# Performance work log

Hardware: AMD Instinct MI355X
Metric: run time of the kernel (lower is better)

Reference implementation:

```python
import jax, jax.numpy as jnp
import numpy as np

B, L, E, V = 4, 2048, 1024, 64
NT = V * (V - 1) // 2  # 2016 upper-triangular entries
LN_EPS = 1e-5


def setup_inputs() -> dict:
    key = jax.random.key(0)
    ks = jax.random.split(key, 9)
    s = lambda d: 1.0 / np.sqrt(d)
    return {
        "hx": jax.random.normal(ks[0], (B, L, E), dtype=jnp.float32),
        "W_dense": jax.random.normal(ks[1], (E, E), dtype=jnp.float32) * s(E),
        "b_dense": jnp.zeros((E,), dtype=jnp.float32),
        "ln_g": jnp.ones((E,), dtype=jnp.float32),
        "ln_b": jnp.zeros((E,), dtype=jnp.float32),
        "W_theta": jax.random.normal(ks[2], (V, E), dtype=jnp.float32) * s(E),
        "b_theta": jnp.zeros((V,), dtype=jnp.float32),
        "W_Theta": jax.random.normal(ks[3], (NT, E), dtype=jnp.float32) * s(E),
        "b_Theta": jnp.zeros((NT,), dtype=jnp.float32),
    }


def reference(hx, W_dense, b_dense, ln_g, ln_b, W_theta, b_theta, W_Theta, b_Theta):
    # dense -> exact (erf) gelu -> LayerNorm (ESM1bLayerNorm)
    h = jax.nn.gelu(hx @ W_dense.T + b_dense, approximate=False)
    mu = jnp.mean(h, axis=-1, keepdims=True)
    var = jnp.mean(jnp.square(h - mu), axis=-1, keepdims=True)
    h = (h - mu) / jnp.sqrt(var + LN_EPS) * ln_g + ln_b

    pi = jax.nn.softmax(h @ W_theta.T + b_theta, axis=-1)          # (B,L,V)
    Theta = jax.nn.softplus(h @ W_Theta.T + b_Theta)               # (B,L,NT)

    iu, ju = np.triu_indices(V, k=1)
    S = jnp.zeros((B, L, V, V), dtype=h.dtype).at[:, :, iu, ju].set(Theta)
    S = S + jnp.swapaxes(S, -2, -1)                                # symmetric, zero diag

    # diag(1/sqrt(pi)) @ S @ diag(sqrt(pi)) == S * sqrt(pi_j)/sqrt(pi_i)
    pi_sqrt = jnp.sqrt(pi)
    Q = S * (pi_sqrt[..., None, :] / pi_sqrt[..., :, None])
    Q = Q - Q.sum(axis=-1)[..., :, None] * jnp.eye(V, dtype=Q.dtype)
    return (Q, pi)
```

## Files before the change

### kernel.cpp

```cpp
#include <hip/hip_runtime.h>
#include <hip/hip_bf16.h>
#include <cstdint>
#include <cstddef>

#define MROWS 8192
#define EDIM  1024
#define VDIM  64
#define NTRI  2016
#define NTC   2176

typedef _Float16 half8  __attribute__((ext_vector_type(8)));
typedef _Float16 half4v __attribute__((ext_vector_type(4)));
typedef float    floatx4 __attribute__((ext_vector_type(4)));

typedef __attribute__((address_space(1))) void gvoid;
typedef __attribute__((address_space(3))) void svoid;

__device__ inline void gld_lds16(const _Float16* g, _Float16* l) {
    __builtin_amdgcn_global_load_lds((gvoid*)g, (svoid*)l, 16, 0, 0);
}

__device__ inline float fast_erf(float x) {
    float ax = fabsf(x);
    float t = 1.0f / (1.0f + 0.3275911f * ax);
    float p = t * (0.254829592f +
              t * (-0.284496736f +
              t * (1.421413741f +
              t * (-1.453152027f +
              t * 1.061405429f))));
    float r = 1.0f - p * __expf(-ax * ax);
    return copysignf(r, x);
}

__device__ inline float fast_softplus(float x) {
    return fmaxf(x, 0.0f) + __logf(1.0f + __expf(-fabsf(x)));
}

__global__ __launch_bounds__(256) void cast_all(const float* __restrict__ hx,
                                                const float* __restrict__ Wd,
                                                const float* __restrict__ WT,
                                                const float* __restrict__ wt,
                                                _Float16* __restrict__ A_h,
                                                _Float16* __restrict__ Wd_h,
                                                _Float16* __restrict__ Wc_h) {
    const int b = blockIdx.x;
    float4 v;
    _Float16* dst;
    int idx;
    if (b < 8192) {
        idx = (b * 256 + threadIdx.x) * 4;
        v = *(const float4*)(hx + idx);
        dst = A_h;
    } else if (b < 9216) {
        idx = ((b - 8192) * 256 + threadIdx.x) * 4;
        v = *(const float4*)(Wd + idx);
        dst = Wd_h;
    } else {
        idx = ((b - 9216) * 256 + threadIdx.x) * 4;
        if (idx < NTRI * EDIM)                  v = *(const float4*)(WT + idx);
        else if (idx < (NTRI + VDIM) * EDIM)    v = *(const float4*)(wt + (idx - NTRI * EDIM));
        else                                    v = make_float4(0.f, 0.f, 0.f, 0.f);
        dst = Wc_h;
    }
    half4v o;
    o[0] = (_Float16)v.x; o[1] = (_Float16)v.y;
    o[2] = (_Float16)v.z; o[3] = (_Float16)v.w;
    *(half4v*)(dst + idx) = o;
}

template <int MODE>
__global__ __launch_bounds__(256, 3) void gemm128(const _Float16* __restrict__ A,
                                                  const _Float16* __restrict__ Bt,
                                                  const float* __restrict__ bias,
                                                  const float* __restrict__ bias2,
                                                  _Float16* __restrict__ C,
                                                  int ldC, int ntg) {
    constexpr int NT = EDIM / 32;
    __shared__ __align__(16) _Float16 S[3][8192];

    const int tid  = threadIdx.x;
    const int xcd  = blockIdx.x & 7;
    const int slot = blockIdx.x >> 3;
    const int mg   = slot / ntg;
    const int nn   = slot - mg * ntg;
    const int m0   = (xcd + mg * 8) * 128;
    const int n0   = nn * 128;

    const int w = tid >> 6, lane = tid & 63;
    const int wr = w >> 1, wc = w & 1;
    const int lrow = lane & 15, lquad = lane >> 4;

    floatx4 acc[4][4] = {};

    const int r0 = tid >> 2;
    const int c0 = tid & 3;
    const int gk = (c0 ^ ((r0 >> 1) & 3)) * 8;
    const _Float16* Ag0 = A  + (size_t)(m0 + r0) * EDIM + gk;
    const _Float16* Ag1 = Ag0 + (size_t)64 * EDIM;
    const _Float16* Bg0 = Bt + (size_t)(n0 + r0) * EDIM + gk;
    const _Float16* Bg1 = Bg0 + (size_t)64 * EDIM;

    const int xr   = (lrow >> 1) & 3;
    const int koff = (lquad ^ xr) * 8;
    const int aoff = (wr * 64 + lrow) * 32 + koff;
    const int boff = 4096 + (wc * 64 + lrow) * 32 + koff;

    auto stage = [&](int buf, int kt) {
        _Float16* d = &S[buf][tid * 8];
        const int ko = kt * 32;
        gld_lds16(Ag0 + ko, d);
        gld_lds16(Ag1 + ko, d + 2048);
        gld_lds16(Bg0 + ko, d + 4096);
        gld_lds16(Bg1 + ko, d + 6144);
    };

    stage(0, 0);
    stage(1, 1);
    asm volatile("s_waitcnt vmcnt(4)" ::: "memory");
    __builtin_amdgcn_s_barrier();

    int buf = 0, sbuf = 2;
#pragma unroll 1
    for (int t = 0; t < NT; ++t) {
        const _Float16* Sb = S[buf];
        if (t + 2 < NT) stage(sbuf, t + 2);

        half8 af[4], bf[4];
#pragma unroll
        for (int i = 0; i < 4; ++i) af[i] = *(const half8*)(Sb + aoff + i * 512);
#pragma unroll
        for (int j = 0; j < 4; ++j) bf[j] = *(const half8*)(Sb + boff + j * 512);

        __builtin_amdgcn_s_setprio(1);
#pragma unroll
        for (int i = 0; i < 4; ++i)
#pragma unroll
            for (int j = 0; j < 4; ++j)
                acc[i][j] = __builtin_amdgcn_mfma_f32_16x16x32_f16(
                    af[i], bf[j], acc[i][j], 0, 0, 0);
        __builtin_amdgcn_s_setprio(0);

        if (t < NT - 2)       asm volatile("s_waitcnt vmcnt(4)" ::: "memory");
        else if (t == NT - 2) asm volatile("s_waitcnt vmcnt(0)" ::: "memory");
        if (t < NT - 1) {
            asm volatile("" ::: "memory");
            __builtin_amdgcn_s_barrier();
            asm volatile("" ::: "memory");
        }
        buf  = (buf  == 2) ? 0 : buf + 1;
        sbuf = (sbuf == 2) ? 0 : sbuf + 1;
    }

    const int cm = m0 + wr * 64 + lquad * 4;
    const int cn = n0 + wc * 64 + lrow;
#pragma unroll
    for (int j = 0; j < 4; ++j) {
        const int gn = cn + j * 16;
        float bv;
        if (MODE == 0) {
            bv = bias[gn];
        } else {
            if (gn < NTRI)             bv = bias[gn];
            else if (gn < NTRI + VDIM) bv = bias2[gn - NTRI];
            else                       bv = 0.0f;
        }
#pragma unroll
        for (int i = 0; i < 4; ++i) {
#pragma unroll
            for (int r = 0; r < 4; ++r) {
                float x = acc[i][j][r] + bv;
                float y;
                if (MODE == 0) {
                    y = 0.5f * x * (1.0f + fast_erf(x * 0.70710678118654752f));
                } else {
                    if (gn < NTRI)             y = fast_softplus(x);
                    else if (gn < NTRI + VDIM) y = x;
                    else                       y = 0.0f;
                }
                C[(size_t)(cm + i * 16 + r) * ldC + gn] = (_Float16)y;
            }
        }
    }
}

__global__ __launch_bounds__(256) void ln_kernel(const _Float16* __restrict__ G,
                                                 const float* __restrict__ gw,
                                                 const float* __restrict__ bw,
                                                 _Float16* __restrict__ Hh) {
    const int row = blockIdx.x, tid = threadIdx.x;
    half4v v = ((const half4v*)(G + (size_t)row * EDIM))[tid];
    float x0 = (float)v[0], x1 = (float)v[1], x2 = (float)v[2], x3 = (float)v[3];
    float s  = x0 + x1 + x2 + x3;
    float ss = x0 * x0 + x1 * x1 + x2 * x2 + x3 * x3;
#pragma unroll
    for (int off = 32; off; off >>= 1) {
        s  += __shfl_down(s, off);
        ss += __shfl_down(ss, off);
    }
    __shared__ float red[8];
    const int w = tid >> 6, lane = tid & 63;
    if (lane == 0) { red[w] = s; red[4 + w] = ss; }
    __syncthreads();
    const float st  = red[0] + red[1] + red[2] + red[3];
    const float sst = red[4] + red[5] + red[6] + red[7];
    const float mu  = st * (1.0f / EDIM);
    const float rs  = 1.0f / sqrtf(sst * (1.0f / EDIM) - mu * mu + 1e-5f);
    float4 gg = ((const float4*)gw)[tid];
    float4 bb = ((const float4*)bw)[tid];
    half4v h4;
    h4[0] = (_Float16)((x0 - mu) * rs * gg.x + bb.x);
    h4[1] = (_Float16)((x1 - mu) * rs * gg.y + bb.y);
    h4[2] = (_Float16)((x2 - mu) * rs * gg.z + bb.z);
    h4[3] = (_Float16)((x3 - mu) * rs * gg.w + bb.w);
    ((half4v*)(Hh + (size_t)row * EDIM))[tid] = h4;
}

__global__ __launch_bounds__(256) void q_kernel(const _Float16* __restrict__ Theta,
                                                float* __restrict__ pi_out,
                                                float* __restrict__ Q) {
    const int row = blockIdx.x;
    const int tid = threadIdx.x;
    __shared__ float Th[NTRI];
    __shared__ float spv[VDIM];
    const _Float16* trow = Theta + (size_t)row * NTC;
    if (tid < 252) {
        half8 h = *(const half8*)(trow + tid * 8);
#pragma unroll
        for (int u = 0; u < 8; ++u) Th[tid * 8 + u] = (float)h[u];
    }
    if (tid >= 192) {
        const int lane = tid & 63;
        float lg = (float)trow[NTRI + lane];
        float m = lg;
#pragma unroll
        for (int off = 32; off; off >>= 1) m = fmaxf(m, __shfl_xor(m, off));
        float e = __expf(lg - m);
        float ssum = e;
#pragma unroll
        for (int off = 32; off; off >>= 1) ssum += __shfl_xor(ssum, off);
        float p = e / ssum;
        pi_out[(size_t)row * VDIM + lane] = p;
        spv[lane] = sqrtf(p);
    }
    __syncthreads();

    const int i = tid >> 2;
    const int q = tid & 3;
    const float rpi = 1.0f / spv[i];
    float vals[16];
    float psum = 0.f;
#pragma unroll
    for (int c = 0; c < 16; ++c) {
        const int j = q * 16 + c;
        float out = 0.f;
        if (j != i) {
            const int a = (i < j) ? i : j;
            const int b = (i < j) ? j : i;
            const int t = a * (127 - a) / 2 + (b - a - 1);
            out = Th[t] * spv[j] * rpi;
            psum += out;
        }
        vals[c] = out;
    }
    psum += __shfl_xor(psum, 1);
    psum += __shfl_xor(psum, 2);
    if ((i >> 4) == q) vals[i & 15] = -psum;

    float* qrow = Q + ((size_t)row * VDIM + i) * VDIM + q * 16;
    float4* dst = (float4*)qrow;
    dst[0] = make_float4(vals[0], vals[1], vals[2], vals[3]);
    dst[1] = make_float4(vals[4], vals[5], vals[6], vals[7]);
    dst[2] = make_float4(vals[8], vals[9], vals[10], vals[11]);
    dst[3] = make_float4(vals[12], vals[13], vals[14], vals[15]);
}

extern "C" void kernel_launch(void* const* d_in, const int* in_sizes, int n_in,
                              void* d_out, int out_size, void* d_ws, size_t ws_size,
                              hipStream_t stream) {
    const float* hx      = (const float*)d_in[0];
    const float* W_dense = (const float*)d_in[1];
    const float* b_dense = (const float*)d_in[2];
    const float* ln_g    = (const float*)d_in[3];
    const float* ln_b    = (const float*)d_in[4];
    const float* W_theta = (const float*)d_in[5];
    const float* b_theta = (const float*)d_in[6];
    const float* W_Theta = (const float*)d_in[7];
    const float* b_Theta = (const float*)d_in[8];

    uint8_t* ws = (uint8_t*)d_ws;
    _Float16* A_h  = (_Float16*)ws;
    _Float16* Wd_h = (_Float16*)(ws + (size_t)16 * 1048576);
    _Float16* Wc_h = (_Float16*)(ws + (size_t)18 * 1048576);
    _Float16* G_h  = (_Float16*)(ws + (size_t)23 * 1048576);
    _Float16* Th_h = (_Float16*)(ws + (size_t)23 * 1048576);

    float* Q_out  = (float*)d_out;
    float* pi_out = (float*)d_out + (size_t)MROWS * VDIM * VDIM;

    cast_all<<<11392, 256, 0, stream>>>(hx, W_dense, W_Theta, W_theta,
                                        A_h, Wd_h, Wc_h);

    gemm128<0><<<512, 256, 0, stream>>>(A_h, Wd_h, b_dense, nullptr, G_h, EDIM, 8);

    ln_kernel<<<MROWS, 256, 0, stream>>>(G_h, ln_g, ln_b, A_h);

    gemm128<1><<<1088, 256, 0, stream>>>(A_h, Wc_h, b_Theta, b_theta, Th_h, NTC, 17);

    q_kernel<<<MROWS, 256, 0, stream>>>(Th_h, pi_out, Q_out);
}
```

Baseline: 307.7 us.

## Replace 128x128 GEMM with 256x128 tile, 8-wave, BK=64 phased pipeline

```diff
diff --git a/kernel.cpp b/kernel.cpp
--- a/kernel.cpp
+++ b/kernel.cpp
@@ -19,6 +19,8 @@
 __device__ inline void gld_lds16(const _Float16* g, _Float16* l) {
     __builtin_amdgcn_global_load_lds((gvoid*)g, (svoid*)l, 16, 0, 0);
 }
+
+#define MFMA16(a, b, c) __builtin_amdgcn_mfma_f32_16x16x32_f16((a), (b), (c), 0, 0, 0)
 
 __device__ inline float fast_erf(float x) {
     float ax = fabsf(x);
@@ -69,92 +71,119 @@
 }
 
 template <int MODE>
-__global__ __launch_bounds__(256, 3) void gemm128(const _Float16* __restrict__ A,
+__global__ __launch_bounds__(512, 2) void gemm256(const _Float16* __restrict__ A,
                                                   const _Float16* __restrict__ Bt,
                                                   const float* __restrict__ bias,
                                                   const float* __restrict__ bias2,
                                                   _Float16* __restrict__ C,
                                                   int ldC, int ntg) {
-    constexpr int NT = EDIM / 32;
-    __shared__ __align__(16) _Float16 S[3][8192];
+    __shared__ __align__(16) _Float16 S[2][24576];
 
     const int tid  = threadIdx.x;
     const int xcd  = blockIdx.x & 7;
     const int slot = blockIdx.x >> 3;
     const int mg   = slot / ntg;
     const int nn   = slot - mg * ntg;
-    const int m0   = (xcd + mg * 8) * 128;
+    const int m0   = (xcd + mg * 8) * 256;
     const int n0   = nn * 128;
 
     const int w = tid >> 6, lane = tid & 63;
-    const int wr = w >> 1, wc = w & 1;
+    const int wr = w >> 2;
+    const int wc = w & 3;
     const int lrow = lane & 15, lquad = lane >> 4;
 
-    floatx4 acc[4][4] = {};
-
-    const int r0 = tid >> 2;
-    const int c0 = tid & 3;
-    const int gk = (c0 ^ ((r0 >> 1) & 3)) * 8;
-    const _Float16* Ag0 = A  + (size_t)(m0 + r0) * EDIM + gk;
-    const _Float16* Ag1 = Ag0 + (size_t)64 * EDIM;
-    const _Float16* Bg0 = Bt + (size_t)(n0 + r0) * EDIM + gk;
-    const _Float16* Bg1 = Bg0 + (size_t)64 * EDIM;
-
-    const int xr   = (lrow >> 1) & 3;
-    const int koff = (lquad ^ xr) * 8;
-    const int aoff = (wr * 64 + lrow) * 32 + koff;
-    const int boff = 4096 + (wc * 64 + lrow) * 32 + koff;
-
-    auto stage = [&](int buf, int kt) {
-        _Float16* d = &S[buf][tid * 8];
-        const int ko = kt * 32;
-        gld_lds16(Ag0 + ko, d);
-        gld_lds16(Ag1 + ko, d + 2048);
-        gld_lds16(Bg0 + ko, d + 4096);
-        gld_lds16(Bg1 + ko, d + 6144);
+    floatx4 acc[8][2] = {};
+
+    const int sr = tid >> 3;
+    const int sc = tid & 7;
+    const int gk = (sc ^ (sr & 7)) * 8;
+    const _Float16* pA = A  + (size_t)(m0 + sr) * EDIM + gk;
+    const _Float16* pB = Bt + (size_t)(n0 + sr) * EDIM + gk;
+
+    const int k0off = ( lquad      ^ (lrow & 7)) * 8;
+    const int k1off = ((4 + lquad) ^ (lrow & 7)) * 8;
+    const int abase = (wr * 128 + lrow) * 64;
+    const int bbase = 16384 + (wc * 32 + lrow) * 64;
+
+    auto stA = [&](int buf, int kt, int seg) {
+        gld_lds16(pA + (size_t)seg * 64 * EDIM + kt * 64,
+                  &S[buf][seg * 4096 + tid * 8]);
     };
-
-    stage(0, 0);
-    stage(1, 1);
-    asm volatile("s_waitcnt vmcnt(4)" ::: "memory");
+    auto stB = [&](int buf, int kt, int seg) {
+        gld_lds16(pB + (size_t)seg * 64 * EDIM + kt * 64,
+                  &S[buf][16384 + seg * 4096 + tid * 8]);
+    };
+
+    half8 bf[4];
+    auto loadB = [&](const _Float16* Sb) {
+        bf[0] = *(const half8*)(Sb + bbase + k0off);
+        bf[1] = *(const half8*)(Sb + bbase + k1off);
+        bf[2] = *(const half8*)(Sb + bbase + 1024 + k0off);
+        bf[3] = *(const half8*)(Sb + bbase + 1024 + k1off);
+    };
+
+#define PHASE(SB, P, STAGE_STMT, TAIL_STMT)                                   \
+    {                                                                         \
+        const _Float16* Sb_ = (SB);                                           \
+        half8 a00 = *(const half8*)(Sb_ + abase + (2*(P))*1024   + k0off);    \
+        half8 a01 = *(const half8*)(Sb_ + abase + (2*(P))*1024   + k1off);    \
+        half8 a10 = *(const half8*)(Sb_ + abase + (2*(P)+1)*1024 + k0off);    \
+        half8 a11 = *(const half8*)(Sb_ + abase + (2*(P)+1)*1024 + k1off);    \
+        STAGE_STMT;                                                           \
+        asm volatile("" ::: "memory");                                        \
+        __builtin_amdgcn_s_barrier();                                         \
+        asm volatile("" ::: "memory");                                        \
+        __builtin_amdgcn_s_setprio(1);                                        \
+        acc[2*(P)][0]   = MFMA16(a00, bf[0], acc[2*(P)][0]);                  \
+        acc[2*(P)][0]   = MFMA16(a01, bf[1], acc[2*(P)][0]);                  \
+        acc[2*(P)][1]   = MFMA16(a00, bf[2], acc[2*(P)][1]);                  \
+        acc[2*(P)][1]   = MFMA16(a01, bf[3], acc[2*(P)][1]);                  \
+        acc[2*(P)+1][0] = MFMA16(a10, bf[0], acc[2*(P)+1][0]);                \
+        acc[2*(P)+1][0] = MFMA16(a11, bf[1], acc[2*(P)+1][0]);                \
+        acc[2*(P)+1][1] = MFMA16(a10, bf[2], acc[2*(P)+1][1]);                \
+        acc[2*(P)+1][1] = MFMA16(a11, bf[3], acc[2*(P)+1][1]);                \
+        __builtin_amdgcn_s_setprio(0);                                        \
+        TAIL_STMT;                                                            \
+        asm volatile("" ::: "memory");                                        \
+        __builtin_amdgcn_s_barrier();                                         \
+        asm volatile("" ::: "memory");                                        \
+    }
+
+    stA(0, 0, 0); stA(0, 0, 1); stA(0, 0, 2); stA(0, 0, 3);
+    stB(0, 0, 0); stB(0, 0, 1);
+    stB(1, 1, 0); stB(1, 1, 1);
+    asm volatile("s_waitcnt vmcnt(2)" ::: "memory");
     __builtin_amdgcn_s_barrier();
-
-    int buf = 0, sbuf = 2;
+    asm volatile("" ::: "memory");
+
 #pragma unroll 1
-    for (int t = 0; t < NT; ++t) {
-        const _Float16* Sb = S[buf];
-        if (t + 2 < NT) stage(sbuf, t + 2);
-
-        half8 af[4], bf[4];
-#pragma unroll
-        for (int i = 0; i < 4; ++i) af[i] = *(const half8*)(Sb + aoff + i * 512);
-#pragma unroll
-        for (int j = 0; j < 4; ++j) bf[j] = *(const half8*)(Sb + boff + j * 512);
-
-        __builtin_amdgcn_s_setprio(1);
-#pragma unroll
-        for (int i = 0; i < 4; ++i)
-#pragma unroll
-            for (int j = 0; j < 4; ++j)
-                acc[i][j] = __builtin_amdgcn_mfma_f32_16x16x32_f16(
-                    af[i], bf[j], acc[i][j], 0, 0, 0);
-        __builtin_amdgcn_s_setprio(0);
-
-        if (t < NT - 2)       asm volatile("s_waitcnt vmcnt(4)" ::: "memory");
-        else if (t == NT - 2) asm volatile("s_waitcnt vmcnt(0)" ::: "memory");
-        if (t < NT - 1) {
-            asm volatile("" ::: "memory");
-            __builtin_amdgcn_s_barrier();
-            asm volatile("" ::: "memory");
-        }
-        buf  = (buf  == 2) ? 0 : buf + 1;
-        sbuf = (sbuf == 2) ? 0 : sbuf + 1;
-    }
-
-    const int cm = m0 + wr * 64 + lquad * 4;
-    const int cn = n0 + wc * 64 + lrow;
-#pragma unroll
-    for (int j = 0; j < 4; ++j) {
+    for (int it = 0; it < 8; ++it) {
+        const int t0 = 2 * it, t1 = 2 * it + 1;
+        const bool st = (it < 7);
+        const _Float16* S0 = S[0];
+        const _Float16* S1 = S[1];
+
+        loadB(S0);
+        PHASE(S0, 0, { stA(1, t1, 0); stA(1, t1, 1); }, {});
+        PHASE(S0, 1, { stA(1, t1, 2); stA(1, t1, 3); }, {});
+        PHASE(S0, 2, { if (st) stB(0, t0 + 2, 0); }, {});
+        PHASE(S0, 3, { if (st) stB(0, t0 + 2, 1); },
+              { if (st) asm volatile("s_waitcnt vmcnt(2)" ::: "memory");
+                else    asm volatile("s_waitcnt vmcnt(0)" ::: "memory"); });
+
+        loadB(S1);
+        PHASE(S1, 0, { if (st) { stA(0, t0 + 2, 0); stA(0, t0 + 2, 1); } }, {});
+        PHASE(S1, 1, { if (st) { stA(0, t0 + 2, 2); stA(0, t0 + 2, 3); } }, {});
+        PHASE(S1, 2, { if (st) stB(1, t1 + 2, 0); }, {});
+        PHASE(S1, 3, { if (st) stB(1, t1 + 2, 1); },
+              { if (st) asm volatile("s_waitcnt vmcnt(2)" ::: "memory"); });
+    }
+#undef PHASE
+
+    const int cm = m0 + wr * 128 + lquad * 4;
+    const int cn = n0 + wc * 32 + lrow;
+#pragma unroll
+    for (int j = 0; j < 2; ++j) {
         const int gn = cn + j * 16;
         float bv;
         if (MODE == 0) {
@@ -165,7 +194,7 @@
             else                       bv = 0.0f;
         }
 #pragma unroll
-        for (int i = 0; i < 4; ++i) {
+        for (int i = 0; i < 8; ++i) {
 #pragma unroll
             for (int r = 0; r < 4; ++r) {
                 float x = acc[i][j][r] + bv;
@@ -300,11 +329,11 @@
     cast_all<<<11392, 256, 0, stream>>>(hx, W_dense, W_Theta, W_theta,
                                         A_h, Wd_h, Wc_h);
 
-    gemm128<0><<<512, 256, 0, stream>>>(A_h, Wd_h, b_dense, nullptr, G_h, EDIM, 8);
+    gemm256<0><<<256, 512, 0, stream>>>(A_h, Wd_h, b_dense, nullptr, G_h, EDIM, 8);
 
     ln_kernel<<<MROWS, 256, 0, stream>>>(G_h, ln_g, ln_b, A_h);
 
-    gemm128<1><<<1088, 256, 0, stream>>>(A_h, Wc_h, b_Theta, b_theta, Th_h, NTC, 17);
+    gemm256<1><<<544, 512, 0, stream>>>(A_h, Wc_h, b_Theta, b_theta, Th_h, NTC, 17);
 
     q_kernel<<<MROWS, 256, 0, stream>>>(Th_h, pi_out, Q_out);
 }
```

New measurement: 314.1 us. 2.1% more time.

## Widen GEMM tiles to 128x256 with 512-thread blocks and mixed-width tail

Applied to the files above, without the earlier changes.

```diff
diff --git a/kernel.cpp b/kernel.cpp
--- a/kernel.cpp
+++ b/kernel.cpp
@@ -19,6 +19,8 @@
 __device__ inline void gld_lds16(const _Float16* g, _Float16* l) {
     __builtin_amdgcn_global_load_lds((gvoid*)g, (svoid*)l, 16, 0, 0);
 }
+
+#define MFMA16(a, b, c) __builtin_amdgcn_mfma_f32_16x16x32_f16((a), (b), (c), 0, 0, 0)
 
 __device__ inline float fast_erf(float x) {
     float ax = fabsf(x);
@@ -68,55 +70,54 @@
     *(half4v*)(dst + idx) = o;
 }
 
-template <int MODE>
-__global__ __launch_bounds__(256, 3) void gemm128(const _Float16* __restrict__ A,
-                                                  const _Float16* __restrict__ Bt,
-                                                  const float* __restrict__ bias,
-                                                  const float* __restrict__ bias2,
-                                                  _Float16* __restrict__ C,
-                                                  int ldC, int ntg) {
+template <int MODE, int BNF>
+__device__ inline void gemm_body(const _Float16* __restrict__ A,
+                                 const _Float16* __restrict__ Bt,
+                                 const float* __restrict__ bias,
+                                 const float* __restrict__ bias2,
+                                 _Float16* __restrict__ C,
+                                 int ldC, int ntg, int bidx, int col0,
+                                 _Float16 (*S)[12288]) {
     constexpr int NT = EDIM / 32;
-    __shared__ __align__(16) _Float16 S[3][8192];
+    constexpr int BN = BNF * 64;
 
     const int tid  = threadIdx.x;
-    const int xcd  = blockIdx.x & 7;
-    const int slot = blockIdx.x >> 3;
+    const int xcd  = bidx & 7;
+    const int slot = bidx >> 3;
     const int mg   = slot / ntg;
     const int nn   = slot - mg * ntg;
     const int m0   = (xcd + mg * 8) * 128;
-    const int n0   = nn * 128;
+    const int n0   = col0 + nn * BN;
 
     const int w = tid >> 6, lane = tid & 63;
-    const int wr = w >> 1, wc = w & 1;
+    const int wr = w >> 2, wc = w & 3;
     const int lrow = lane & 15, lquad = lane >> 4;
 
-    floatx4 acc[4][4] = {};
+    floatx4 acc[4][BNF] = {};
 
     const int r0 = tid >> 2;
     const int c0 = tid & 3;
     const int gk = (c0 ^ ((r0 >> 1) & 3)) * 8;
-    const _Float16* Ag0 = A  + (size_t)(m0 + r0) * EDIM + gk;
-    const _Float16* Ag1 = Ag0 + (size_t)64 * EDIM;
+    const _Float16* Ag  = A  + (size_t)(m0 + r0) * EDIM + gk;
     const _Float16* Bg0 = Bt + (size_t)(n0 + r0) * EDIM + gk;
-    const _Float16* Bg1 = Bg0 + (size_t)64 * EDIM;
+    const _Float16* Bg1 = Bg0 + (size_t)128 * EDIM;
 
     const int xr   = (lrow >> 1) & 3;
     const int koff = (lquad ^ xr) * 8;
     const int aoff = (wr * 64 + lrow) * 32 + koff;
-    const int boff = 4096 + (wc * 64 + lrow) * 32 + koff;
+    const int boff = 4096 + (wc * (BNF * 16) + lrow) * 32 + koff;
 
     auto stage = [&](int buf, int kt) {
-        _Float16* d = &S[buf][tid * 8];
         const int ko = kt * 32;
-        gld_lds16(Ag0 + ko, d);
-        gld_lds16(Ag1 + ko, d + 2048);
-        gld_lds16(Bg0 + ko, d + 4096);
-        gld_lds16(Bg1 + ko, d + 6144);
+        gld_lds16(Ag + ko, &S[buf][tid * 8]);
+        gld_lds16(Bg0 + ko, &S[buf][4096 + tid * 8]);
+        if constexpr (BNF == 4) gld_lds16(Bg1 + ko, &S[buf][8192 + tid * 8]);
     };
 
     stage(0, 0);
     stage(1, 1);
-    asm volatile("s_waitcnt vmcnt(4)" ::: "memory");
+    if constexpr (BNF == 4) asm volatile("s_waitcnt vmcnt(3)" ::: "memory");
+    else                    asm volatile("s_waitcnt vmcnt(2)" ::: "memory");
     __builtin_amdgcn_s_barrier();
 
     int buf = 0, sbuf = 2;
@@ -125,23 +126,26 @@
         const _Float16* Sb = S[buf];
         if (t + 2 < NT) stage(sbuf, t + 2);
 
-        half8 af[4], bf[4];
-#pragma unroll
-        for (int i = 0; i < 4; ++i) af[i] = *(const half8*)(Sb + aoff + i * 512);
-#pragma unroll
-        for (int j = 0; j < 4; ++j) bf[j] = *(const half8*)(Sb + boff + j * 512);
+        half8 af[4], bf[BNF];
+#pragma unroll
+        for (int i = 0; i < 4; ++i)   af[i] = *(const half8*)(Sb + aoff + i * 512);
+#pragma unroll
+        for (int j = 0; j < BNF; ++j) bf[j] = *(const half8*)(Sb + boff + j * 512);
 
         __builtin_amdgcn_s_setprio(1);
 #pragma unroll
         for (int i = 0; i < 4; ++i)
 #pragma unroll
-            for (int j = 0; j < 4; ++j)
-                acc[i][j] = __builtin_amdgcn_mfma_f32_16x16x32_f16(
-                    af[i], bf[j], acc[i][j], 0, 0, 0);
+            for (int j = 0; j < BNF; ++j)
+                acc[i][j] = MFMA16(af[i], bf[j], acc[i][j]);
         __builtin_amdgcn_s_setprio(0);
 
-        if (t < NT - 2)       asm volatile("s_waitcnt vmcnt(4)" ::: "memory");
-        else if (t == NT - 2) asm volatile("s_waitcnt vmcnt(0)" ::: "memory");
+        if (t < NT - 2) {
+            if constexpr (BNF == 4) asm volatile("s_waitcnt vmcnt(3)" ::: "memory");
+            else                    asm volatile("s_waitcnt vmcnt(2)" ::: "memory");
+        } else if (t == NT - 2) {
+            asm volatile("s_waitcnt vmcnt(0)" ::: "memory");
+        }
         if (t < NT - 1) {
             asm volatile("" ::: "memory");
             __builtin_amdgcn_s_barrier();
@@ -152,9 +156,9 @@
     }
 
     const int cm = m0 + wr * 64 + lquad * 4;
-    const int cn = n0 + wc * 64 + lrow;
-#pragma unroll
-    for (int j = 0; j < 4; ++j) {
+    const int cn = n0 + wc * (BNF * 16) + lrow;
+#pragma unroll
+    for (int j = 0; j < BNF; ++j) {
         const int gn = cn + j * 16;
         float bv;
         if (MODE == 0) {
@@ -180,6 +184,23 @@
                 C[(size_t)(cm + i * 16 + r) * ldC + gn] = (_Float16)y;
             }
         }
+    }
+}
+
+template <int MODE>
+__global__ __launch_bounds__(512, 4) void gemmw(const _Float16* __restrict__ A,
+                                                const _Float16* __restrict__ Bt,
+                                                const float* __restrict__ bias,
+                                                const float* __restrict__ bias2,
+                                                _Float16* __restrict__ C,
+                                                int ldC, int ntgW, int nwide,
+                                                int ntgN, int col0N) {
+    __shared__ __align__(16) _Float16 S[3][12288];
+    if ((int)blockIdx.x < nwide) {
+        gemm_body<MODE, 4>(A, Bt, bias, bias2, C, ldC, ntgW, blockIdx.x, 0, S);
+    } else {
+        gemm_body<MODE, 2>(A, Bt, bias, bias2, C, ldC, ntgN,
+                           blockIdx.x - nwide, col0N, S);
     }
 }
 
@@ -300,11 +321,13 @@
     cast_all<<<11392, 256, 0, stream>>>(hx, W_dense, W_Theta, W_theta,
                                         A_h, Wd_h, Wc_h);
 
-    gemm128<0><<<512, 256, 0, stream>>>(A_h, Wd_h, b_dense, nullptr, G_h, EDIM, 8);
+    gemmw<0><<<256, 512, 0, stream>>>(A_h, Wd_h, b_dense, nullptr, G_h,
+                                      EDIM, 4, 256, 0, 0);
 
     ln_kernel<<<MROWS, 256, 0, stream>>>(G_h, ln_g, ln_b, A_h);
 
-    gemm128<1><<<1088, 256, 0, stream>>>(A_h, Wc_h, b_Theta, b_theta, Th_h, NTC, 17);
+    gemmw<1><<<576, 512, 0, stream>>>(A_h, Wc_h, b_Theta, b_theta, Th_h,
+                                      NTC, 8, 512, 1, 2048);
 
     q_kernel<<<MROWS, 256, 0, stream>>>(Th_h, pi_out, Q_out);
 }
```

New measurement: 304.3 us. About the same (-1.1%).
